# Kernel tuning notes

Hardware: AMD Instinct MI355X
Metric: run time of the kernel (lower is better)

## Reference

```python
import jax, jax.numpy as jnp
import numpy as np

MIN_V, MAX_V = 1e-7, 10.0
POWER = 2.0
N_NODES = 200000


def _hyper_layer(H, edges, W, b):
    """One HyperTensorGraphConvolution layer (full-neighborhood branch).

    H: [N, d] node signals; edges: [E, S] node indices per hyperedge.
    For each (edge, node_i): power-mean over the other S-1 nodes of the edge,
    divided by (S-1), accumulated onto node_i; then row-normalize and linear.
    """
    N, d = H.shape
    E, S = edges.shape
    H = jnp.clip(H, MIN_V, MAX_V)
    P = H ** POWER                                   # [N, d]
    g = P[edges]                                     # [E, S, d] gather
    edge_sum = g.sum(axis=1, keepdims=True)          # [E, 1, d]
    neigh_mean = (edge_sum - g) / (S - 1)            # exclude self, /(len(nodes)-1)
    contrib = neigh_mean ** (1.0 / POWER)            # [E, S, d]
    add = jax.ops.segment_sum(contrib.reshape(E * S, d),
                              edges.reshape(-1), num_segments=N)
    new_signal = H + add
    # row-normalize (rowsum > 0 because H >= 1e-7)
    rowsum = new_signal.sum(axis=1)
    r_inv = jnp.where(jnp.isfinite(1.0 / rowsum), 1.0 / rowsum, 0.0)
    AH = new_signal * r_inv[:, None]
    return AH @ W + b


def setup_inputs() -> dict:
    key = jax.random.key(0)
    k1, k2, k3, k4, k5, k6 = jax.random.split(key, 6)
    d, h, c = 128, 16, 40
    H = jax.random.uniform(k1, (N_NODES, d), dtype=jnp.float32)
    edges = jax.random.randint(k2, (40000, 16), 0, N_NODES, dtype=jnp.int64)
    std1 = 1.0 / np.sqrt(h)
    std2 = 1.0 / np.sqrt(c)
    W1 = jax.random.uniform(k3, (d, h), jnp.float32, -std1, std1)
    b1 = jax.random.uniform(k4, (h,), jnp.float32, -std1, std1)
    W2 = jax.random.uniform(k5, (h, c), jnp.float32, -std2, std2)
    b2 = jax.random.uniform(k6, (c,), jnp.float32, -std2, std2)
    return {"H": H, "W1": W1, "b1": b1, "W2": W2, "b2": b2, "edges": edges}


def reference(H, W1, b1, W2, b2, edges):
    # layer 1 + relu (dropout is identity in eval mode)
    x = jax.nn.relu(_hyper_layer(H, edges, W1, b1))
    # layer 2
    return _hyper_layer(x, edges, W2, b2)
```

## Files before the change

kernel.cpp:

```cpp
#include <hip/hip_runtime.h>

#define MIN_V 1e-7f
#define MAX_V 10.0f
#define INV15 (1.0f/15.0f)
#define CAP 32

typedef _Float16 half2v __attribute__((ext_vector_type(2)));
typedef _Float16 half4v __attribute__((ext_vector_type(4)));
typedef _Float16 half8v __attribute__((ext_vector_type(8)));

static __device__ __forceinline__ float clipv(float v){
    return fminf(fmaxf(v, MIN_V), MAX_V);
}
static __device__ __forceinline__ half2v shflx1(half2v v){
    int i = __builtin_bit_cast(int, v);
    i = __shfl_xor(i, 1, 64);
    return __builtin_bit_cast(half2v, i);
}

__global__ __launch_bounds__(256) void ch_stream(const float* __restrict__ H,
                                                 _Float16* __restrict__ CH, int total8){
    int stride = gridDim.x*256;
    for (int i = blockIdx.x*256 + threadIdx.x; i < total8; i += stride){
        const float4* p = (const float4*)(H + (size_t)i*8);
        float4 a = p[0], b = p[1];
        half8v o;
        o[0]=(_Float16)clipv(a.x); o[1]=(_Float16)clipv(a.y);
        o[2]=(_Float16)clipv(a.z); o[3]=(_Float16)clipv(a.w);
        o[4]=(_Float16)clipv(b.x); o[5]=(_Float16)clipv(b.y);
        o[6]=(_Float16)clipv(b.z); o[7]=(_Float16)clipv(b.w);
        *(half8v*)(CH + (size_t)i*8) = o;
    }
}

__global__ void build_lists(const int* __restrict__ edges, int* __restrict__ cnt,
                            unsigned short* __restrict__ lists, int total){
    int i = blockIdx.x*256 + threadIdx.x;
    if (i >= total) return;
    int node = edges[i];
    int p = atomicAdd(&cnt[node], 1);
    if (p < CAP) lists[(size_t)node*CAP + p] = (unsigned short)(i >> 4);
}

__global__ __launch_bounds__(256) void es_l1(const _Float16* __restrict__ CH,
                                             const int* __restrict__ edges,
                                             _Float16* __restrict__ ES1s, int E){
    int tid = threadIdx.x;
    int sub = tid & 15;
    int e = blockIdx.x*16 + (tid >> 4);
    if (e >= E) return;
    int nid = edges[(size_t)e*16 + sub];
    float s[8];
    #pragma unroll
    for (int j=0;j<8;++j) s[j] = 0.f;
    #pragma unroll
    for (int t=0;t<16;++t){
        int idx = __shfl(nid, t, 16);
        half8v v = *(const half8v*)(CH + (size_t)idx*128 + sub*8);
        #pragma unroll
        for (int j=0;j<8;++j){ float f = (float)v[j]; s[j] += f*f; }
    }
    half8v o;
    #pragma unroll
    for (int j=0;j<8;++j) o[j] = (_Float16)(s[j]*INV15);
    *(half8v*)(ES1s + (size_t)e*128 + sub*8) = o;
}

__global__ __launch_bounds__(256) void fused_l1(
    const _Float16* __restrict__ CH, const _Float16* __restrict__ ES1s,
    const int* __restrict__ cnt, const unsigned short* __restrict__ lists,
    const float* __restrict__ W1, const float* __restrict__ b1,
    _Float16* __restrict__ X, int N, int EZERO){
    __shared__ _Float16 snw[2][8*128];
    int tid = threadIdx.x;
    int wave = tid >> 6, lane = tid & 63;

    int q = lane >> 4, h = lane & 15;
    half2v w2[16];
    #pragma unroll
    for (int i=0;i<16;++i){
        w2[i][0] = (_Float16)W1[(q*32+2*i  )*16 + h];
        w2[i][1] = (_Float16)W1[(q*32+2*i+1)*16 + h];
    }
    const half2v ones = {(_Float16)1.f, (_Float16)1.f};
    float bv = b1[h];

    int hw = tid >> 5;
    int k32 = tid & 31;
    int dq = k32 * 4;

    const _Float16 i15 = (_Float16)INV15;
    const half4v i15v = {i15, i15, i15, i15};
    const half4v z4 = {(_Float16)0.f,(_Float16)0.f,(_Float16)0.f,(_Float16)0.f};

    int nchunks = (N + 7) >> 3;
    int parity = 0;
    for (int chunk = blockIdx.x; chunk < nchunks; chunk += gridDim.x, parity ^= 1){
        int nb = chunk * 8;
        _Float16* sbuf = &snw[parity][0];

        int n = nb + hw;
        if (n < N){
            int len = cnt[n]; if (len > CAP) len = CAP;
            int myid = (int)lists[(size_t)n*CAP + k32];
            myid = (k32 < len) ? myid : EZERO;

            half4v hv = *(const half4v*)(CH + (size_t)n*128 + dq);
            half4v p16 = (hv * hv) * i15v;

            float a0=0.f, a1=0.f, a2=0.f, a3=0.f;
            for (int k0=0;k0<len;k0+=8){
                half4v v[8];
                #pragma unroll
                for (int j=0;j<8;++j){
                    int e = __shfl(myid, k0+j, 32);
                    v[j] = *(const half4v*)(ES1s + (size_t)e*128 + dq);
                }
                #pragma unroll
                for (int j=0;j<8;++j){
                    half4v sq = __builtin_elementwise_sqrt(__builtin_elementwise_max(v[j] - p16, z4));
                    a0 += (float)sq[0];
                    a1 += (float)sq[1];
                    a2 += (float)sq[2];
                    a3 += (float)sq[3];
                }
            }
            half4v o;
            o[0] = (_Float16)((float)hv[0] + a0);
            o[1] = (_Float16)((float)hv[1] + a1);
            o[2] = (_Float16)((float)hv[2] + a2);
            o[3] = (_Float16)((float)hv[3] + a3);
            *(half4v*)&sbuf[hw*128 + dq] = o;
        }
        __syncthreads();

        #pragma unroll
        for (int r=0;r<2;++r){
            int nl = wave*2 + r;
            int n2 = nb + nl;
            if (n2 >= N) continue;
            float acc = 0.f, rs = 0.f;
            #pragma unroll
            for (int j=0;j<8;++j){
                half4v v = *(const half4v*)&sbuf[nl*128 + q*32 + j*4];
                half2v lo = {v[0], v[1]}, hi = {v[2], v[3]};
                acc = __builtin_amdgcn_fdot2(lo, w2[j*2  ], acc, false);
                acc = __builtin_amdgcn_fdot2(hi, w2[j*2+1], acc, false);
                rs  = __builtin_amdgcn_fdot2(lo, ones, rs, false);
                rs  = __builtin_amdgcn_fdot2(hi, ones, rs, false);
            }
            acc += __shfl_xor(acc, 16, 64);
            rs  += __shfl_xor(rs , 16, 64);
            acc += __shfl_xor(acc, 32, 64);
            rs  += __shfl_xor(rs , 32, 64);
            if (q == 0){
                float o = acc * __builtin_amdgcn_rcpf(rs) + bv;
                X[(size_t)n2*16 + h] = (_Float16)fmaxf(o, 0.f);
            }
        }
    }
}

__global__ __launch_bounds__(256) void es_l2(const _Float16* __restrict__ X,
                                             const int* __restrict__ edges,
                                             _Float16* __restrict__ ES2s, int E){
    int t = blockIdx.x*256 + threadIdx.x;
    int e = t >> 2, dq = (t & 3)*4;
    if (e >= E) return;
    const int* row = edges + (size_t)e*16;
    const _Float16 c7 = (_Float16)1e-7f;
    const half4v c7v = {c7, c7, c7, c7};
    float s0=0.f, s1=0.f, s2=0.f, s3=0.f;
    #pragma unroll
    for (int s=0;s<16;++s){
        half4v v = *(const half4v*)(X + (size_t)row[s]*16 + dq);
        v = __builtin_elementwise_max(v, c7v);
        float f0=(float)v[0], f1=(float)v[1], f2=(float)v[2], f3=(float)v[3];
        s0 += f0*f0; s1 += f1*f1; s2 += f2*f2; s3 += f3*f3;
    }
    half4v o;
    o[0]=(_Float16)(s0*INV15); o[1]=(_Float16)(s1*INV15);
    o[2]=(_Float16)(s2*INV15); o[3]=(_Float16)(s3*INV15);
    *(half4v*)(ES2s + (size_t)e*16 + dq) = o;
}

__global__ __launch_bounds__(256) void node_l2(
    const _Float16* __restrict__ X, const _Float16* __restrict__ ES2s,
    const int* __restrict__ cnt, const unsigned short* __restrict__ lists,
    const float* __restrict__ W2, const float* __restrict__ b2,
    float* __restrict__ out, int N, int EZERO){
    __shared__ half2v sW2h[8*40];
    __shared__ float sb[40];
    for (int i=threadIdx.x;i<320;i+=256){
        int d2 = i/40, c = i - d2*40;
        half2v wp;
        wp[0] = (_Float16)W2[(2*d2  )*40 + c];
        wp[1] = (_Float16)W2[(2*d2+1)*40 + c];
        sW2h[i] = wp;
    }
    if (threadIdx.x < 40) sb[threadIdx.x] = b2[threadIdx.x];
    __syncthreads();
    int t = blockIdx.x*256 + threadIdx.x;
    int n = t >> 1, p = t & 1;
    if (n >= N) return;

    const _Float16 c7 = (_Float16)1e-7f;
    const half8v c7v = {c7,c7,c7,c7,c7,c7,c7,c7};
    const half8v z8 = {(_Float16)0.f,(_Float16)0.f,(_Float16)0.f,(_Float16)0.f,
                       (_Float16)0.f,(_Float16)0.f,(_Float16)0.f,(_Float16)0.f};
    const _Float16 i15 = (_Float16)INV15;
    const half8v i15v = {i15,i15,i15,i15,i15,i15,i15,i15};

    half8v xh = *(const half8v*)(X + (size_t)n*16 + p*8);
    xh = __builtin_elementwise_max(xh, c7v);
    half8v ps = (xh*xh)*i15v;

    float xc[8], ad[8];
    #pragma unroll
    for (int d=0;d<8;++d){ xc[d]=(float)xh[d]; ad[d]=0.f; }

    int len = cnt[n]; if (len > CAP) len = CAP;
    const unsigned short* lrow = lists + (size_t)n*CAP;
    for (int k0=0;k0<len;k0+=4){
        int e0 = (int)lrow[k0];
        int e1 = (k0+1 < len) ? (int)lrow[k0+1] : EZERO;
        int e2 = (k0+2 < len) ? (int)lrow[k0+2] : EZERO;
        int e3 = (k0+3 < len) ? (int)lrow[k0+3] : EZERO;
        half8v r0 = *(const half8v*)(ES2s + (size_t)e0*16 + p*8);
        half8v r1 = *(const half8v*)(ES2s + (size_t)e1*16 + p*8);
        half8v r2 = *(const half8v*)(ES2s + (size_t)e2*16 + p*8);
        half8v r3 = *(const half8v*)(ES2s + (size_t)e3*16 + p*8);
        half8v s0 = __builtin_elementwise_sqrt(__builtin_elementwise_max(r0-ps, z8));
        half8v s1 = __builtin_elementwise_sqrt(__builtin_elementwise_max(r1-ps, z8));
        half8v s2 = __builtin_elementwise_sqrt(__builtin_elementwise_max(r2-ps, z8));
        half8v s3 = __builtin_elementwise_sqrt(__builtin_elementwise_max(r3-ps, z8));
        #pragma unroll
        for (int d=0;d<8;++d)
            ad[d] += ((float)s0[d] + (float)s1[d]) + ((float)s2[d] + (float)s3[d]);
    }
    float rsl = 0.f;
    float nw[8];
    #pragma unroll
    for (int d=0;d<8;++d){ nw[d] = xc[d] + ad[d]; rsl += nw[d]; }
    float rs = rsl + __shfl_xor(rsl, 1, 64);
    float rinv = __builtin_amdgcn_rcpf(rs);

    half2v mine[4], oth[4];
    #pragma unroll
    for (int i=0;i<4;++i){
        mine[i][0] = (_Float16)nw[2*i];
        mine[i][1] = (_Float16)nw[2*i+1];
        oth[i] = shflx1(mine[i]);
    }
    half2v all8[8];
    #pragma unroll
    for (int i=0;i<4;++i){
        all8[4*p + i]     = mine[i];
        all8[4*(1-p) + i] = oth[i];
    }

    float ob[20];
    #pragma unroll
    for (int c=0;c<20;++c){
        int col = p*20 + c;
        float acc = 0.f;
        #pragma unroll
        for (int d2=0;d2<8;++d2)
            acc = __builtin_amdgcn_fdot2(all8[d2], sW2h[d2*40+col], acc, false);
        ob[c] = rinv*acc + sb[col];
    }
    float4* op = (float4*)(out + (size_t)n*40 + p*20);
    #pragma unroll
    for (int j=0;j<5;++j) op[j] = ((float4*)ob)[j];
}

extern "C" void kernel_launch(void* const* d_in, const int* in_sizes, int n_in,
                              void* d_out, int out_size, void* d_ws, size_t ws_size,
                              hipStream_t stream){
    (void)n_in; (void)out_size; (void)ws_size;
    const float* H  = (const float*)d_in[0];
    const float* W1 = (const float*)d_in[1];
    const float* b1 = (const float*)d_in[2];
    const float* W2 = (const float*)d_in[3];
    const float* b2 = (const float*)d_in[4];
    const int* edges = (const int*)d_in[5];
    float* out = (float*)d_out;

    const int N = in_sizes[0] / 128;
    const int E = in_sizes[5] / 16;
    const int total = E * 16;
    const int total8 = N * 128 / 8;

    char* ws = (char*)d_ws;
    size_t off = 0;
    _Float16* CH   = (_Float16*)(ws + off);
    _Float16* ES2s = (_Float16*)(ws + off);
    off += (size_t)N*128*sizeof(_Float16);
    _Float16* ES1s = (_Float16*)(ws + off); off += (size_t)(E+1)*128*sizeof(_Float16);
    _Float16* X    = (_Float16*)(ws + off); off += (size_t)N*16*sizeof(_Float16);
    int* cnt = (int*)(ws + off); off += (size_t)N*sizeof(int);
    unsigned short* lists = (unsigned short*)(ws + off);
    off += (size_t)N*CAP*sizeof(unsigned short);

    hipMemsetAsync(cnt, 0, (size_t)N*sizeof(int), stream);
    hipMemsetAsync(ES1s + (size_t)E*128, 0, 128*sizeof(_Float16), stream);
    ch_stream<<<2048, 256, 0, stream>>>(H, CH, total8);
    build_lists<<<(total+255)/256, 256, 0, stream>>>(edges, cnt, lists, total);
    es_l1<<<(E+15)/16, 256, 0, stream>>>(CH, edges, ES1s, E);
    fused_l1<<<2048, 256, 0, stream>>>(CH, ES1s, cnt, lists, W1, b1, X, N, E);
    hipMemsetAsync(ES2s + (size_t)E*16, 0, 16*sizeof(_Float16), stream);
    es_l2<<<(E*4+255)/256, 256, 0, stream>>>(X, edges, ES2s, E);
    node_l2<<<(N*2+255)/256, 256, 0, stream>>>(X, ES2s, cnt, lists, W2, b2, out, N, E);
}
```

Baseline: 210.0 us.

## Prefill adjacency lists with sentinel and load edge ids as vectors

The conversion kernel now also fills every adjacency list slot with the zero-edge sentinel. Gather loops can then read four edge ids with one vector load and need no per-slot bounds selects or cross-lane shuffles. The es_l1 kernel reads edge indices directly instead of shuffling them, and the layer-1 projection reads shared memory in 8-wide chunks. The fill adds N*64 bytes of extra writes.

```diff
diff --git a/kernel.cpp b/kernel.cpp
--- a/kernel.cpp
+++ b/kernel.cpp
@@ -8,6 +8,7 @@
 typedef _Float16 half2v __attribute__((ext_vector_type(2)));
 typedef _Float16 half4v __attribute__((ext_vector_type(4)));
 typedef _Float16 half8v __attribute__((ext_vector_type(8)));
+typedef unsigned short ushort4v __attribute__((ext_vector_type(4)));
 
 static __device__ __forceinline__ float clipv(float v){
     return fminf(fmaxf(v, MIN_V), MAX_V);
@@ -18,8 +19,10 @@
     return __builtin_bit_cast(half2v, i);
 }
 
-__global__ __launch_bounds__(256) void ch_stream(const float* __restrict__ H,
-                                                 _Float16* __restrict__ CH, int total8){
+__global__ __launch_bounds__(256) void ch_fill(const float* __restrict__ H,
+                                               _Float16* __restrict__ CH,
+                                               unsigned* __restrict__ lists32,
+                                               unsigned pat, int total8){
     int stride = gridDim.x*256;
     for (int i = blockIdx.x*256 + threadIdx.x; i < total8; i += stride){
         const float4* p = (const float4*)(H + (size_t)i*8);
@@ -30,6 +33,7 @@
         o[4]=(_Float16)clipv(b.x); o[5]=(_Float16)clipv(b.y);
         o[6]=(_Float16)clipv(b.z); o[7]=(_Float16)clipv(b.w);
         *(half8v*)(CH + (size_t)i*8) = o;
+        lists32[i] = pat;
     }
 }
 
@@ -49,13 +53,13 @@
     int sub = tid & 15;
     int e = blockIdx.x*16 + (tid >> 4);
     if (e >= E) return;
-    int nid = edges[(size_t)e*16 + sub];
+    const int* row = edges + (size_t)e*16;
     float s[8];
     #pragma unroll
     for (int j=0;j<8;++j) s[j] = 0.f;
     #pragma unroll
     for (int t=0;t<16;++t){
-        int idx = __shfl(nid, t, 16);
+        int idx = row[t];
         half8v v = *(const half8v*)(CH + (size_t)idx*128 + sub*8);
         #pragma unroll
         for (int j=0;j<8;++j){ float f = (float)v[j]; s[j] += f*f; }
@@ -70,7 +74,7 @@
     const _Float16* __restrict__ CH, const _Float16* __restrict__ ES1s,
     const int* __restrict__ cnt, const unsigned short* __restrict__ lists,
     const float* __restrict__ W1, const float* __restrict__ b1,
-    _Float16* __restrict__ X, int N, int EZERO){
+    _Float16* __restrict__ X, int N){
     __shared__ _Float16 snw[2][8*128];
     int tid = threadIdx.x;
     int wave = tid >> 6, lane = tid & 63;
@@ -102,28 +106,26 @@
         int n = nb + hw;
         if (n < N){
             int len = cnt[n]; if (len > CAP) len = CAP;
-            int myid = (int)lists[(size_t)n*CAP + k32];
-            myid = (k32 < len) ? myid : EZERO;
+            const unsigned short* lrow = lists + (size_t)n*CAP;
 
             half4v hv = *(const half4v*)(CH + (size_t)n*128 + dq);
             half4v p16 = (hv * hv) * i15v;
 
             float a0=0.f, a1=0.f, a2=0.f, a3=0.f;
-            for (int k0=0;k0<len;k0+=8){
-                half4v v[8];
-                #pragma unroll
-                for (int j=0;j<8;++j){
-                    int e = __shfl(myid, k0+j, 32);
-                    v[j] = *(const half4v*)(ES1s + (size_t)e*128 + dq);
-                }
-                #pragma unroll
-                for (int j=0;j<8;++j){
-                    half4v sq = __builtin_elementwise_sqrt(__builtin_elementwise_max(v[j] - p16, z4));
-                    a0 += (float)sq[0];
-                    a1 += (float)sq[1];
-                    a2 += (float)sq[2];
-                    a3 += (float)sq[3];
-                }
+            for (int k0=0;k0<len;k0+=4){
+                ushort4v e4 = *(const ushort4v*)(lrow + k0);
+                half4v v0 = *(const half4v*)(ES1s + (size_t)e4[0]*128 + dq);
+                half4v v1 = *(const half4v*)(ES1s + (size_t)e4[1]*128 + dq);
+                half4v v2 = *(const half4v*)(ES1s + (size_t)e4[2]*128 + dq);
+                half4v v3 = *(const half4v*)(ES1s + (size_t)e4[3]*128 + dq);
+                half4v s0 = __builtin_elementwise_sqrt(__builtin_elementwise_max(v0 - p16, z4));
+                half4v s1 = __builtin_elementwise_sqrt(__builtin_elementwise_max(v1 - p16, z4));
+                half4v s2 = __builtin_elementwise_sqrt(__builtin_elementwise_max(v2 - p16, z4));
+                half4v s3 = __builtin_elementwise_sqrt(__builtin_elementwise_max(v3 - p16, z4));
+                a0 += ((float)s0[0] + (float)s1[0]) + ((float)s2[0] + (float)s3[0]);
+                a1 += ((float)s0[1] + (float)s1[1]) + ((float)s2[1] + (float)s3[1]);
+                a2 += ((float)s0[2] + (float)s1[2]) + ((float)s2[2] + (float)s3[2]);
+                a3 += ((float)s0[3] + (float)s1[3]) + ((float)s2[3] + (float)s3[3]);
             }
             half4v o;
             o[0] = (_Float16)((float)hv[0] + a0);
@@ -141,13 +143,17 @@
             if (n2 >= N) continue;
             float acc = 0.f, rs = 0.f;
             #pragma unroll
-            for (int j=0;j<8;++j){
-                half4v v = *(const half4v*)&sbuf[nl*128 + q*32 + j*4];
-                half2v lo = {v[0], v[1]}, hi = {v[2], v[3]};
-                acc = __builtin_amdgcn_fdot2(lo, w2[j*2  ], acc, false);
-                acc = __builtin_amdgcn_fdot2(hi, w2[j*2+1], acc, false);
-                rs  = __builtin_amdgcn_fdot2(lo, ones, rs, false);
-                rs  = __builtin_amdgcn_fdot2(hi, ones, rs, false);
+            for (int j=0;j<4;++j){
+                half8v v = *(const half8v*)&sbuf[nl*128 + q*32 + j*8];
+                half2v p0 = {v[0],v[1]}, p1 = {v[2],v[3]}, p2 = {v[4],v[5]}, p3 = {v[6],v[7]};
+                acc = __builtin_amdgcn_fdot2(p0, w2[j*4+0], acc, false);
+                acc = __builtin_amdgcn_fdot2(p1, w2[j*4+1], acc, false);
+                acc = __builtin_amdgcn_fdot2(p2, w2[j*4+2], acc, false);
+                acc = __builtin_amdgcn_fdot2(p3, w2[j*4+3], acc, false);
+                rs  = __builtin_amdgcn_fdot2(p0, ones, rs, false);
+                rs  = __builtin_amdgcn_fdot2(p1, ones, rs, false);
+                rs  = __builtin_amdgcn_fdot2(p2, ones, rs, false);
+                rs  = __builtin_amdgcn_fdot2(p3, ones, rs, false);
             }
             acc += __shfl_xor(acc, 16, 64);
             rs  += __shfl_xor(rs , 16, 64);
@@ -188,7 +194,7 @@
     const _Float16* __restrict__ X, const _Float16* __restrict__ ES2s,
     const int* __restrict__ cnt, const unsigned short* __restrict__ lists,
     const float* __restrict__ W2, const float* __restrict__ b2,
-    float* __restrict__ out, int N, int EZERO){
+    float* __restrict__ out, int N){
     __shared__ half2v sW2h[8*40];
     __shared__ float sb[40];
     for (int i=threadIdx.x;i<320;i+=256){
@@ -222,14 +228,11 @@
     int len = cnt[n]; if (len > CAP) len = CAP;
     const unsigned short* lrow = lists + (size_t)n*CAP;
     for (int k0=0;k0<len;k0+=4){
-        int e0 = (int)lrow[k0];
-        int e1 = (k0+1 < len) ? (int)lrow[k0+1] : EZERO;
-        int e2 = (k0+2 < len) ? (int)lrow[k0+2] : EZERO;
-        int e3 = (k0+3 < len) ? (int)lrow[k0+3] : EZERO;
-        half8v r0 = *(const half8v*)(ES2s + (size_t)e0*16 + p*8);
-        half8v r1 = *(const half8v*)(ES2s + (size_t)e1*16 + p*8);
-        half8v r2 = *(const half8v*)(ES2s + (size_t)e2*16 + p*8);
-        half8v r3 = *(const half8v*)(ES2s + (size_t)e3*16 + p*8);
+        ushort4v e4 = *(const ushort4v*)(lrow + k0);
+        half8v r0 = *(const half8v*)(ES2s + (size_t)e4[0]*16 + p*8);
+        half8v r1 = *(const half8v*)(ES2s + (size_t)e4[1]*16 + p*8);
+        half8v r2 = *(const half8v*)(ES2s + (size_t)e4[2]*16 + p*8);
+        half8v r3 = *(const half8v*)(ES2s + (size_t)e4[3]*16 + p*8);
         half8v s0 = __builtin_elementwise_sqrt(__builtin_elementwise_max(r0-ps, z8));
         half8v s1 = __builtin_elementwise_sqrt(__builtin_elementwise_max(r1-ps, z8));
         half8v s2 = __builtin_elementwise_sqrt(__builtin_elementwise_max(r2-ps, z8));
@@ -302,13 +305,14 @@
     unsigned short* lists = (unsigned short*)(ws + off);
     off += (size_t)N*CAP*sizeof(unsigned short);
 
+    unsigned pat = (unsigned)E | ((unsigned)E << 16);
     hipMemsetAsync(cnt, 0, (size_t)N*sizeof(int), stream);
     hipMemsetAsync(ES1s + (size_t)E*128, 0, 128*sizeof(_Float16), stream);
-    ch_stream<<<2048, 256, 0, stream>>>(H, CH, total8);
+    ch_fill<<<2048, 256, 0, stream>>>(H, CH, (unsigned*)lists, pat, total8);
     build_lists<<<(total+255)/256, 256, 0, stream>>>(edges, cnt, lists, total);
     es_l1<<<(E+15)/16, 256, 0, stream>>>(CH, edges, ES1s, E);
-    fused_l1<<<2048, 256, 0, stream>>>(CH, ES1s, cnt, lists, W1, b1, X, N, E);
+    fused_l1<<<2048, 256, 0, stream>>>(CH, ES1s, cnt, lists, W1, b1, X, N);
     hipMemsetAsync(ES2s + (size_t)E*16, 0, 16*sizeof(_Float16), stream);
     es_l2<<<(E*4+255)/256, 256, 0, stream>>>(X, edges, ES2s, E);
-    node_l2<<<(N*2+255)/256, 256, 0, stream>>>(X, ES2s, cnt, lists, W2, b2, out, N, E);
-}
+    node_l2<<<(N*2+255)/256, 256, 0, stream>>>(X, ES2s, cnt, lists, W2, b2, out, N);
+}
```

Measured after the change: 212.6 us. No clear change (+1.2%).

## Use one block per 8-node chunk in fused_l1 with fp16 accumulation

Applied to the files above, without the earlier changes.

Replaces the grid-stride persistent loop in fused_l1 with a launch of one block per 8-node chunk and drops the double-buffered shared memory. The gather loop now issues 4 loads per step instead of 8 and accumulates in a packed half4 vector instead of four fp32 scalars. This removes the per-block W1 reload amortisation and lowers register pressure, which may raise occupancy. The fp16 accumulation over up to 32 terms loses precision relative to the fp32 sums.

```diff
diff --git a/kernel.cpp b/kernel.cpp
--- a/kernel.cpp
+++ b/kernel.cpp
@@ -71,7 +71,7 @@
     const int* __restrict__ cnt, const unsigned short* __restrict__ lists,
     const float* __restrict__ W1, const float* __restrict__ b1,
     _Float16* __restrict__ X, int N, int EZERO){
-    __shared__ _Float16 snw[2][8*128];
+    __shared__ _Float16 snw[8*128];
     int tid = threadIdx.x;
     int wave = tid >> 6, lane = tid & 63;
 
@@ -88,75 +88,62 @@
     int hw = tid >> 5;
     int k32 = tid & 31;
     int dq = k32 * 4;
+    int nb = blockIdx.x * 8;
 
     const _Float16 i15 = (_Float16)INV15;
     const half4v i15v = {i15, i15, i15, i15};
     const half4v z4 = {(_Float16)0.f,(_Float16)0.f,(_Float16)0.f,(_Float16)0.f};
 
-    int nchunks = (N + 7) >> 3;
-    int parity = 0;
-    for (int chunk = blockIdx.x; chunk < nchunks; chunk += gridDim.x, parity ^= 1){
-        int nb = chunk * 8;
-        _Float16* sbuf = &snw[parity][0];
-
-        int n = nb + hw;
-        if (n < N){
-            int len = cnt[n]; if (len > CAP) len = CAP;
-            int myid = (int)lists[(size_t)n*CAP + k32];
-            myid = (k32 < len) ? myid : EZERO;
-
-            half4v hv = *(const half4v*)(CH + (size_t)n*128 + dq);
-            half4v p16 = (hv * hv) * i15v;
-
-            float a0=0.f, a1=0.f, a2=0.f, a3=0.f;
-            for (int k0=0;k0<len;k0+=8){
-                half4v v[8];
-                #pragma unroll
-                for (int j=0;j<8;++j){
-                    int e = __shfl(myid, k0+j, 32);
-                    v[j] = *(const half4v*)(ES1s + (size_t)e*128 + dq);
-                }
-                #pragma unroll
-                for (int j=0;j<8;++j){
-                    half4v sq = __builtin_elementwise_sqrt(__builtin_elementwise_max(v[j] - p16, z4));
-                    a0 += (float)sq[0];
-                    a1 += (float)sq[1];
-                    a2 += (float)sq[2];
-                    a3 += (float)sq[3];
-                }
-            }
-            half4v o;
-            o[0] = (_Float16)((float)hv[0] + a0);
-            o[1] = (_Float16)((float)hv[1] + a1);
-            o[2] = (_Float16)((float)hv[2] + a2);
-            o[3] = (_Float16)((float)hv[3] + a3);
-            *(half4v*)&sbuf[hw*128 + dq] = o;
+    int n = nb + hw;
+    if (n < N){
+        int len = cnt[n]; if (len > CAP) len = CAP;
+        int myid = (int)lists[(size_t)n*CAP + k32];
+        myid = (k32 < len) ? myid : EZERO;
+
+        half4v hv = *(const half4v*)(CH + (size_t)n*128 + dq);
+        half4v p16 = (hv * hv) * i15v;
+
+        half4v acc = z4;
+        for (int k0=0;k0<len;k0+=4){
+            int e0 = __shfl(myid, k0,   32);
+            int e1 = __shfl(myid, k0+1, 32);
+            int e2 = __shfl(myid, k0+2, 32);
+            int e3 = __shfl(myid, k0+3, 32);
+            half4v v0 = *(const half4v*)(ES1s + (size_t)e0*128 + dq);
+            half4v v1 = *(const half4v*)(ES1s + (size_t)e1*128 + dq);
+            half4v v2 = *(const half4v*)(ES1s + (size_t)e2*128 + dq);
+            half4v v3 = *(const half4v*)(ES1s + (size_t)e3*128 + dq);
+            acc = acc + __builtin_elementwise_sqrt(__builtin_elementwise_max(v0 - p16, z4));
+            acc = acc + __builtin_elementwise_sqrt(__builtin_elementwise_max(v1 - p16, z4));
+            acc = acc + __builtin_elementwise_sqrt(__builtin_elementwise_max(v2 - p16, z4));
+            acc = acc + __builtin_elementwise_sqrt(__builtin_elementwise_max(v3 - p16, z4));
         }
-        __syncthreads();
-
+        *(half4v*)&snw[hw*128 + dq] = hv + acc;
+    }
+    __syncthreads();
+
+    #pragma unroll
+    for (int r=0;r<2;++r){
+        int nl = wave*2 + r;
+        int n2 = nb + nl;
+        if (n2 >= N) continue;
+        float acc = 0.f, rs = 0.f;
         #pragma unroll
-        for (int r=0;r<2;++r){
-            int nl = wave*2 + r;
-            int n2 = nb + nl;
-            if (n2 >= N) continue;
-            float acc = 0.f, rs = 0.f;
-            #pragma unroll
-            for (int j=0;j<8;++j){
-                half4v v = *(const half4v*)&sbuf[nl*128 + q*32 + j*4];
-                half2v lo = {v[0], v[1]}, hi = {v[2], v[3]};
-                acc = __builtin_amdgcn_fdot2(lo, w2[j*2  ], acc, false);
-                acc = __builtin_amdgcn_fdot2(hi, w2[j*2+1], acc, false);
-                rs  = __builtin_amdgcn_fdot2(lo, ones, rs, false);
-                rs  = __builtin_amdgcn_fdot2(hi, ones, rs, false);
-            }
-            acc += __shfl_xor(acc, 16, 64);
-            rs  += __shfl_xor(rs , 16, 64);
-            acc += __shfl_xor(acc, 32, 64);
-            rs  += __shfl_xor(rs , 32, 64);
-            if (q == 0){
-                float o = acc * __builtin_amdgcn_rcpf(rs) + bv;
-                X[(size_t)n2*16 + h] = (_Float16)fmaxf(o, 0.f);
-            }
+        for (int j=0;j<8;++j){
+            half4v v = *(const half4v*)&snw[nl*128 + q*32 + j*4];
+            half2v lo = {v[0], v[1]}, hi = {v[2], v[3]};
+            acc = __builtin_amdgcn_fdot2(lo, w2[j*2  ], acc, false);
+            acc = __builtin_amdgcn_fdot2(hi, w2[j*2+1], acc, false);
+            rs  = __builtin_amdgcn_fdot2(lo, ones, rs, false);
+            rs  = __builtin_amdgcn_fdot2(hi, ones, rs, false);
+        }
+        acc += __shfl_xor(acc, 16, 64);
+        rs  += __shfl_xor(rs , 16, 64);
+        acc += __shfl_xor(acc, 32, 64);
+        rs  += __shfl_xor(rs , 32, 64);
+        if (q == 0){
+            float o = acc * __builtin_amdgcn_rcpf(rs) + bv;
+            X[(size_t)n2*16 + h] = (_Float16)fmaxf(o, 0.f);
         }
     }
 }
@@ -307,7 +294,7 @@
     ch_stream<<<2048, 256, 0, stream>>>(H, CH, total8);
     build_lists<<<(total+255)/256, 256, 0, stream>>>(edges, cnt, lists, total);
     es_l1<<<(E+15)/16, 256, 0, stream>>>(CH, edges, ES1s, E);
-    fused_l1<<<2048, 256, 0, stream>>>(CH, ES1s, cnt, lists, W1, b1, X, N, E);
+    fused_l1<<<(N+7)/8, 256, 0, stream>>>(CH, ES1s, cnt, lists, W1, b1, X, N, E);
     hipMemsetAsync(ES2s + (size_t)E*16, 0, 16*sizeof(_Float16), stream);
     es_l2<<<(E*4+255)/256, 256, 0, stream>>>(X, edges, ES2s, E);
     node_l2<<<(N*2+255)/256, 256, 0, stream>>>(X, ES2s, cnt, lists, W2, b2, out, N, E);
```

Measured after the change: 197.3 us (median of 2 runs). 1.06x faster.
